# Kernel tuning notes

Measured on AMD Instinct MI355X. Metric: run time of the kernel, lower is better.

Reference implementation:

```python
import jax, jax.numpy as jnp
import numpy as np


def _pick(key, nodes, mask, cnt):
    # Uniformly pick one of the `cnt` entries of `nodes` where mask is True.
    r = jax.random.randint(key, (), 0, jnp.maximum(cnt, 1))
    cs = jnp.cumsum(mask.astype(jnp.int32))
    return nodes[jnp.argmax(cs == r + 1)]


def _one_walk(key, nbrs, f0, n_faces, L):
    # nbrs: [N,3] int32 neighbor table, f0: scalar start face.
    seq = jnp.zeros((L + 1,), jnp.int32).at[0].set(f0)
    visited = jnp.zeros((n_faces + 1,), bool).at[n_faces].set(True).at[f0].set(True)

    def cond(st):
        return st[2] <= L

    def body(st):
        seq, visited, i, bs, k = st
        k, k1, k2, k3 = jax.random.split(k, 4)
        cur = seq[i - 1]
        nb = nbrs[cur]                     # [3] neighbor candidates
        unv = ~visited[nb]
        cnt = unv.sum()
        need = cnt == 0                    # stuck -> backtrack
        cand = _pick(k1, nb, unv, cnt)

        def bcond(c):
            bs_c, found = c[0], c[1]
            return need & (~found) & (i > bs_c)

        def bbody(c):
            bs_c, found, ta, kk = c
            kk, kp = jax.random.split(kk)
            back = seq[i - bs_c - 1]
            bn = nbrs[back]
            bm = ~visited[bn]
            bc = bm.sum()
            f2 = bc > 0
            ta2 = _pick(kp, bn, bm, bc)
            return (jnp.where(f2, bs_c, bs_c + 2), f2, jnp.where(f2, ta2, ta), kk)

        bs_f, found, ta_bt, _ = jax.lax.while_loop(
            bcond, bbody, (bs, jnp.array(False), jnp.int32(0), k2))
        rand_node = jax.random.randint(k3, (), 0, n_faces, dtype=jnp.int32)
        to_add = jnp.where(~need, cand, jnp.where(found, ta_bt, rand_node))
        hit = need & found                 # successful backtrack
        bs_new = jnp.where(hit, bs_f, jnp.int32(1))
        i_new = jnp.where(hit, i - bs_f, i)
        ar = jnp.arange(L + 1, dtype=jnp.int32)
        # torch: replace seq[i-bs:i] with to_add on successful backtrack
        seq = jnp.where(hit & (ar >= i_new) & (ar < i), to_add, seq)
        visited = visited.at[to_add].set(True)
        seq = seq.at[i_new].set(to_add)
        return (seq, visited, i_new + 1, bs_new, k)

    seq, *_ = jax.lax.while_loop(
        cond, body, (seq, visited, jnp.int32(1), jnp.int32(1), key))
    return seq


def patch_random_walk(key, neighbors, centers, n_faces, seq_len):
    B, G = centers.shape
    keys = jax.random.split(key, B * G).reshape(B, G)
    walk_g = jax.vmap(_one_walk, in_axes=(0, None, 0, None, None))
    walk_bg = jax.vmap(walk_g, in_axes=(0, 0, 0, None, None))
    return walk_bg(keys, neighbors, centers, n_faces, seq_len)  # [B,G,L+1] int32


def setup_inputs() -> dict:
    key = jax.random.key(0)
    k1, k2, k3 = jax.random.split(key, 3)
    B, N, G = 4, 20000, 1024
    xyz = jax.random.normal(k1, (B, N, 3), dtype=jnp.float32)
    neighbors = jax.random.randint(k2, (B, N, 3), 0, N, dtype=jnp.int32)
    centers = jax.random.randint(k3, (B, G), 0, N, dtype=jnp.int32)
    return {"xyz": xyz, "neighbors": neighbors, "centers": centers,
            "n_faces": N, "seq_len": 63}


def reference(xyz, neighbors, centers, n_faces, seq_len):
    # patch_random_walk -> idx [B,G,K]; then Group.forward gather + recenter.
    idx = patch_random_walk(jax.random.key(42), neighbors, centers, n_faces, seq_len)
    gather = jax.vmap(lambda p, i: p[i])(xyz, idx)            # [B,G,K,3]
    center_xyz = jax.vmap(lambda p, c: p[c])(xyz, centers)    # [B,G,3]
    return gather - center_xyz[:, :, None, :]
```

## Files before the change

### kernel.cpp

```cpp
#include <hip/hip_runtime.h>
#include <stdint.h>
#include <stddef.h>


namespace {

__device__ __forceinline__ uint32_t rotl32(uint32_t x, int r) {
  return (x << r) | (x >> (32 - r));
}

__device__ __forceinline__ void tf2x32(uint32_t ka, uint32_t kb,
                                       uint32_t x0, uint32_t x1,
                                       uint32_t& o0, uint32_t& o1) {
  const uint32_t kc = ka ^ kb ^ 0x1BD11BDAu;
  x0 += ka; x1 += kb;
#define TF_R4(r0, r1, r2, r3)                          \
  x0 += x1; x1 = rotl32(x1, r0); x1 ^= x0;             \
  x0 += x1; x1 = rotl32(x1, r1); x1 ^= x0;             \
  x0 += x1; x1 = rotl32(x1, r2); x1 ^= x0;             \
  x0 += x1; x1 = rotl32(x1, r3); x1 ^= x0;
  TF_R4(13, 15, 26, 6)  x0 += kb; x1 += kc + 1u;
  TF_R4(17, 29, 16, 24) x0 += kc; x1 += ka + 2u;
  TF_R4(13, 15, 26, 6)  x0 += ka; x1 += kb + 3u;
  TF_R4(17, 29, 16, 24) x0 += kb; x1 += kc + 4u;
  TF_R4(13, 15, 26, 6)  x0 += kc; x1 += ka + 5u;
#undef TF_R4
  o0 = x0; o1 = x1;
}

__device__ __forceinline__ void randbits(uint32_t ka, uint32_t kb,
                                         uint32_t& hi, uint32_t& lo) {
  uint32_t s0a, s0b, s1a, s1b, h0, h1;
  tf2x32(ka, kb, 0u, 0u, s0a, s0b);
  tf2x32(ka, kb, 0u, 1u, s1a, s1b);
  tf2x32(s0a, s0b, 0u, 0u, h0, h1);
  hi = h0 ^ h1;
  tf2x32(s1a, s1b, 0u, 0u, h0, h1);
  lo = h0 ^ h1;
}

__device__ __forceinline__ uint32_t r_generic(uint32_t hi, uint32_t lo,
                                              uint32_t span) {
  uint32_t mult = 65536u % span;
  mult = (mult * mult) % span;
  return ((hi % span) * mult + (lo % span)) % span;
}

__device__ __forceinline__ uint32_t pick_code(uint32_t hi, uint32_t lo) {
  return ((hi % 3u + lo % 3u) % 3u) | ((lo & 1u) << 2);
}

constexpr int WPB = 16;
constexpr int CH = 64;
constexpr int NMAX = 20000;
constexpr int VISW = 625;
constexpr int THREADS = 512;

__global__ __launch_bounds__(512) void walk_kernel(
    const float* __restrict__ xyz, const int* __restrict__ nbrs,
    const int* __restrict__ centers, const int* __restrict__ n_faces_p,
    const int* __restrict__ seq_len_p, float* __restrict__ out,
    int s0, int num_walks, int Lp1) {
  __shared__ uint32_t nb01L[NMAX];
  __shared__ uint16_t nb2L[NMAX];
  __shared__ __align__(16) uint32_t visL[WPB * VISW];
  __shared__ uint16_t seqL[WPB][CH + 4];
  __shared__ float cenL[WPB][3];

  const int tid = threadIdx.x;
  const int wv = tid >> 6, lane = tid & 63;
  const int w0 = blockIdx.x * WPB;
  if (w0 >= num_walks) return;

  const int N = *n_faces_p;
  const int L = *seq_len_p;
  const int B = s0 / (3 * N);
  const int G = num_walks / B;
  const bool lds_ok = (N <= NMAX) && (G % WPB == 0) && (L < CH);
  const int bb0 = w0 / G;

  if (wv == 0) {
    if (lane < WPB && (w0 + lane) < num_walks) {
      uint32_t ka, kb;
      tf2x32(0u, 42u, 0u, (uint32_t)(w0 + lane), ka, kb);
      visL[(lane * CH + 0) * 2 + 0] = ka;
      visL[(lane * CH + 0) * 2 + 1] = kb;
#pragma clang loop unroll(disable)
      for (int c2 = 1; c2 < CH; ++c2) {
        tf2x32(ka, kb, 0u, 0u, ka, kb);
        visL[(lane * CH + c2) * 2 + 0] = ka;
        visL[(lane * CH + c2) * 2 + 1] = kb;
      }
    }
  } else if (lds_ok) {
    const int* __restrict__ nbT = nbrs + (size_t)bb0 * N * 3;
    for (int r = tid - 64; r < N; r += (THREADS - 64)) {
      const int3 v = *reinterpret_cast<const int3*>(nbT + 3 * (size_t)r);
      nb01L[r] = (uint32_t)v.x | ((uint32_t)v.y << 16);
      nb2L[r]  = (uint16_t)v.z;
    }
  }
  __syncthreads();

  if (lds_ok) {
    const float* __restrict__ xb = xyz + (size_t)bb0 * N * 3;
    uint8_t* const codesB = reinterpret_cast<uint8_t*>(&visL[2048]);
#pragma unroll
    for (int p = 0; p < (WPB * CH) / THREADS; ++p) {
      const int pair = tid + THREADS * p;
      const int wk = pair >> 6, st = pair & 63;
      if ((w0 + wk) < num_walks) {
        const uint32_t ka = visL[(wk * CH + st) * 2 + 0];
        const uint32_t kb = visL[(wk * CH + st) * 2 + 1];
        uint32_t k1a, k1b, hi, lo;
        tf2x32(ka, kb, 0u, 1u, k1a, k1b);
        randbits(k1a, k1b, hi, lo);
        codesB[wk * CH + st] = (uint8_t)pick_code(hi, lo);
      }
    }
    if (tid < WPB && (w0 + tid) < num_walks) {
      const int f0t = centers[w0 + tid];
      cenL[tid][0] = xb[3 * (size_t)f0t + 0];
      cenL[tid][1] = xb[3 * (size_t)f0t + 1];
      cenL[tid][2] = xb[3 * (size_t)f0t + 2];
    }
    __syncthreads();

    const int kw = 2 * wv + (lane >> 5);
    const int w = w0 + kw;
    const bool walker = ((lane & 31) == 0) && (w < num_walks);
    uint32_t cw[7] = {0, 0, 0, 0, 0, 0, 0};
    uint32_t k0a = 0, k0b = 0;
    if (walker) {
      tf2x32(0u, 42u, 0u, (uint32_t)w, k0a, k0b);
      const uint32_t* cwd = &visL[2048 + kw * (CH / 4)];
#pragma unroll
      for (int t = 0; t < CH / 4; ++t) {
        const uint32_t wd = cwd[t];
#pragma unroll
        for (int b = 0; b < 4; ++b) {
          const int s = 4 * t + b;
          const uint32_t c3 = (wd >> (8 * b)) & 7u;
          cw[s / 10] |= c3 << (3 * (s % 10));
        }
      }
    }
    __syncthreads();
    {
      uint4* const v4 = reinterpret_cast<uint4*>(visL);
      const uint4 z = make_uint4(0u, 0u, 0u, 0u);
      for (int j = tid; j < (WPB * VISW) / 4; j += THREADS) v4[j] = z;
    }
    __syncthreads();

    const int f0 = walker ? centers[w] : 0;
    uint32_t* __restrict__ visW = visL + (walker ? kw : 0) * VISW;

    if (walker) {
      visW[(unsigned)f0 >> 5] = 1u << (f0 & 31);
      seqL[kw][0] = (uint16_t)f0;
    }

    const uint32_t p0 = nb01L[f0];
    int n0 = (int)(p0 & 0xffffu), n1 = (int)(p0 >> 16), n2 = (int)nb2L[f0];
    uint32_t wd0 = visW[(unsigned)n0 >> 5];
    uint32_t wd1 = visW[(unsigned)n1 >> 5];
    uint32_t wd2 = visW[(unsigned)n2 >> 5];
    uint32_t pA01, pB01, pC01, pA2, pB2, pC2;

    int extc = 0; uint32_t extka = k0a, extkb = k0b;
    int c = 0, bs = 1;
    int i = L + 1;
    bool do_general = true;

    if (L == 63) {
      uint32_t sticky = 0u;
      uint32_t sp[32];
#pragma unroll
      for (int j = 0; j < 32; ++j) sp[j] = 0u;
      sp[0] = (uint32_t)f0 & 0xffffu;
#pragma clang loop unroll(full)
      for (int cc = 0; cc < 63; ++cc) {
        const uint32_t u0 = ((wd0 >> (n0 & 31)) & 1u) ^ 1u;
        const uint32_t u1 = ((wd1 >> (n1 & 31)) & 1u) ^ 1u;
        const uint32_t u2 = ((wd2 >> (n2 & 31)) & 1u) ^ 1u;
        const uint32_t cnt = u0 + u1 + u2;
        sticky |= (cnt == 0u) ? 1u : 0u;
        const uint32_t code = (cw[cc / 10] >> (3 * (cc % 10))) & 7u;
        const uint32_t r3 = code & 3u, r2 = (code >> 2) & 1u;
        const uint32_t tgt = (cnt == 3u ? r3 : (cnt == 2u ? r2 : 0u)) + 1u;
        const int sel = (u0 == tgt) ? 0 : ((u0 + u1 == tgt) ? 1 : 2);
        const int to_add = (sel == 0) ? n0 : ((sel == 1) ? n1 : n2);
        const uint32_t wsel = (sel == 0) ? wd0 : ((sel == 1) ? wd1 : wd2);
        if (walker) {
          visW[(unsigned)to_add >> 5] = wsel | (1u << (to_add & 31));
        }
        sp[(cc + 1) >> 1] |= (uint32_t)to_add << (16 * ((cc + 1) & 1));
        const uint32_t pr01 = nb01L[to_add];
        const uint32_t pr2v = nb2L[to_add];
        n0 = (int)(pr01 & 0xffffu); n1 = (int)(pr01 >> 16); n2 = (int)pr2v;
        wd0 = visW[(unsigned)n0 >> 5];
        wd1 = visW[(unsigned)n1 >> 5];
        wd2 = visW[(unsigned)n2 >> 5];
      }
      if (walker) {
        uint32_t* rowp = reinterpret_cast<uint32_t*>(&seqL[kw][0]);
#pragma unroll
        for (int j = 0; j < 32; ++j) rowp[j] = sp[j];
      }
      const bool redo = walker && (sticky != 0u);
      if (__builtin_expect(__any(redo), 0)) {
        if (redo) {
          for (int j = 0; j < VISW; ++j) visW[j] = 0u;
          visW[(unsigned)f0 >> 5] = 1u << (f0 & 31);
          seqL[kw][0] = (uint16_t)f0;
        }
        i = redo ? 1 : (L + 1);
        c = 0; bs = 1;
        const uint32_t pr0 = nb01L[f0];
        const uint32_t pr2v = nb2L[f0];
        if (redo) {
          n0 = (int)(pr0 & 0xffffu); n1 = (int)(pr0 >> 16); n2 = (int)pr2v;
        }
      } else {
        do_general = false;
      }
    } else {
      i = walker ? 1 : (L + 1);
    }

    if (do_general) {
      pA01 = nb01L[n0]; pA2 = nb2L[n0];
      pB01 = nb01L[n1]; pB2 = nb2L[n1];
      pC01 = nb01L[n2]; pC2 = nb2L[n2];
      wd0 = visW[(unsigned)n0 >> 5];
      wd1 = visW[(unsigned)n1 >> 5];
      wd2 = visW[(unsigned)n2 >> 5];
      for (;; ++c) {
        if (!__any(i <= L)) break;
        const bool act = (i <= L);

        const uint32_t u0 = ((wd0 >> (n0 & 31)) & 1u) ^ 1u;
        const uint32_t u1 = ((wd1 >> (n1 & 31)) & 1u) ^ 1u;
        const uint32_t u2 = ((wd2 >> (n2 & 31)) & 1u) ^ 1u;
        const uint32_t cnt = u0 + u1 + u2;

        uint32_t code;
        if (__builtin_expect(c < CH, 1)) {
          const int wi = c / 10;
          const int sh = 3 * (c - wi * 10);
          uint32_t cwv = cw[0];
          cwv = (wi == 1) ? cw[1] : cwv;  cwv = (wi == 2) ? cw[2] : cwv;
          cwv = (wi == 3) ? cw[3] : cwv;  cwv = (wi == 4) ? cw[4] : cwv;
          cwv = (wi == 5) ? cw[5] : cwv;  cwv = (wi == 6) ? cw[6] : cwv;
          code = (cwv >> sh) & 7u;
        } else {
          while (extc < c) { tf2x32(extka, extkb, 0u, 0u, extka, extkb); ++extc; }
          uint32_t k1a, k1b, hi, lo;
          tf2x32(extka, extkb, 0u, 1u, k1a, k1b);
          randbits(k1a, k1b, hi, lo);
          code = pick_code(hi, lo);
        }

        const bool need = act && (cnt == 0u);
        if (__builtin_expect(__any(need), 0)) {
          while (extc < c) { tf2x32(extka, extkb, 0u, 0u, extka, extkb); ++extc; }
          const uint32_t kia = extka, kib = extkb;
          bool found = false; int ta = 0; int bsc = bs;
          if (need) {
            uint32_t kka, kkb;
            tf2x32(kia, kib, 0u, 2u, kka, kkb);
            while (!found && i > bsc) {
              uint32_t ca, cb, kpa, kpb;
              tf2x32(kka, kkb, 0u, 0u, ca, cb);
              tf2x32(kka, kkb, 0u, 1u, kpa, kpb);
              const int back = (int)seqL[kw][i - bsc - 1];
              const uint32_t pm = nb01L[back];
              const int m0 = (int)(pm & 0xffffu), m1 = (int)(pm >> 16);
              const int m2 = (int)nb2L[back];
              const uint32_t e0 = ((visW[(unsigned)m0 >> 5] >> (m0 & 31)) & 1u) ^ 1u;
              const uint32_t e1 = ((visW[(unsigned)m1 >> 5] >> (m1 & 31)) & 1u) ^ 1u;
              const uint32_t e2 = ((visW[(unsigned)m2 >> 5] >> (m2 & 31)) & 1u) ^ 1u;
              const uint32_t bc = e0 + e1 + e2;
              if (bc > 0) {
                uint32_t bhi, blo;
                randbits(kpa, kpb, bhi, blo);
                const uint32_t bcode = pick_code(bhi, blo);
                const uint32_t br3 = bcode & 3u, br2 = (bcode >> 2) & 1u;
                const uint32_t t2v = (bc == 3 ? br3 : (bc == 2 ? br2 : 0)) + 1;
                ta = (e0 == t2v) ? m0 : ((e0 + e1 == t2v) ? m1 : m2);
                found = true;
              } else {
                bsc += 2;
              }
              kka = ca; kkb = cb;
            }
          }
          int rnd = 0;
          if (need && !found) {
            uint32_t k3a, k3b, rhi, rlo;
            tf2x32(kia, kib, 0u, 3u, k3a, k3b);
            randbits(k3a, k3b, rhi, rlo);
            rnd = (int)r_generic(rhi, rlo, (uint32_t)N);
          }
          const uint32_t r3 = code & 3u, r2 = (code >> 2) & 1u;
          const uint32_t tgt = (cnt == 3 ? r3 : (cnt == 2 ? r2 : 0)) + 1;
          const int selc = (u0 == tgt) ? 0 : ((u0 + u1 == tgt) ? 1 : 2);
          const int to_add_c = (selc == 0) ? n0 : ((selc == 1) ? n1 : n2);
          const uint32_t wselc = (selc == 0) ? wd0 : ((selc == 1) ? wd1 : wd2);

          const bool hit = need && found;
          const int to_add = need ? (found ? ta : rnd) : to_add_c;

          if (act) {
            uint32_t wdf = need ? visW[(unsigned)to_add >> 5] : wselc;
            visW[(unsigned)to_add >> 5] = wdf | (1u << (to_add & 31));
            if (hit) {
              const int i_new = i - bsc;
              for (int j = i_new; j < i; ++j) seqL[kw][j] = (uint16_t)to_add;
              bs = bsc; i = i_new + 1;
            } else {
              seqL[kw][i] = (uint16_t)to_add;
              bs = 1; ++i;
            }
          }
          const int rn = act ? to_add : 0;
          const uint32_t pr = nb01L[rn];
          const uint32_t pr2 = nb2L[rn];
          if (act) {
            n0 = (int)(pr & 0xffffu); n1 = (int)(pr >> 16); n2 = (int)pr2;
          }
        } else {
          const uint32_t r3 = code & 3u, r2 = (code >> 2) & 1u;
          const uint32_t tgt = (cnt == 3 ? r3 : (cnt == 2 ? r2 : 0)) + 1;
          const int sel = (u0 == tgt) ? 0 : ((u0 + u1 == tgt) ? 1 : 2);
          const int to_add = (sel == 0) ? n0 : ((sel == 1) ? n1 : n2);
          const uint32_t wsel = (sel == 0) ? wd0 : ((sel == 1) ? wd1 : wd2);
          if (act) {
            visW[(unsigned)to_add >> 5] = wsel | (1u << (to_add & 31));
            seqL[kw][i] = (uint16_t)to_add;
            bs = 1; ++i;
            if (sel == 0)      { n0 = (int)(pA01 & 0xffffu); n1 = (int)(pA01 >> 16); n2 = (int)pA2; }
            else if (sel == 1) { n0 = (int)(pB01 & 0xffffu); n1 = (int)(pB01 >> 16); n2 = (int)pB2; }
            else               { n0 = (int)(pC01 & 0xffffu); n1 = (int)(pC01 >> 16); n2 = (int)pC2; }
          }
        }
        pA01 = nb01L[n0]; pA2 = nb2L[n0];
        pB01 = nb01L[n1]; pB2 = nb2L[n1];
        pC01 = nb01L[n2]; pC2 = nb2L[n2];
        wd0 = visW[(unsigned)n0 >> 5];
        wd1 = visW[(unsigned)n1 >> 5];
        wd2 = visW[(unsigned)n2 >> 5];
      }
    }

    __syncthreads();

    const int items = WPB * Lp1;
    for (int idx = tid; idx < items; idx += THREADS) {
      const int wl = idx / Lp1;
      const int p = idx - wl * Lp1;
      const int ww = w0 + wl;
      if (ww < num_walks) {
        const int node = (int)seqL[wl][p];
        const float* xr = xb + 3 * (size_t)node;
        float3 v;
        v.x = xr[0] - cenL[wl][0];
        v.y = xr[1] - cenL[wl][1];
        v.z = xr[2] - cenL[wl][2];
        *reinterpret_cast<float3*>(out + ((size_t)ww * Lp1 + p) * 3) = v;
      }
    }
  } else {
    for (int sub = 0; sub < 2; ++sub) {
      const int w = w0 + 2 * wv + sub;
      if (w >= num_walks) continue;
      const int bb = w / G;
      const int* __restrict__ nbG = nbrs + (size_t)bb * N * 3;
      const float* __restrict__ xb = xyz + (size_t)bb * N * 3;
      const int f0 = centers[w];
      const uint32_t mka = visL[((2 * wv + sub) * CH + lane) * 2 + 0];
      const uint32_t mkb = visL[((2 * wv + sub) * CH + lane) * 2 + 1];
      uint32_t mycode;
      {
        uint32_t k1a, k1b, hi, lo;
        tf2x32(mka, mkb, 0u, 1u, k1a, k1b);
        randbits(k1a, k1b, hi, lo);
        mycode = pick_code(hi, lo);
      }
      uint32_t extka = 0, extkb = 0;
      int extc = -1;
      auto get_key = [&](int idxk, uint32_t& ra, uint32_t& rb) {
        if (idxk < CH) {
          ra = (uint32_t)__shfl((int)mka, idxk);
          rb = (uint32_t)__shfl((int)mkb, idxk);
        } else {
          if (extc < 0) {
            extka = (uint32_t)__shfl((int)mka, CH - 1);
            extkb = (uint32_t)__shfl((int)mkb, CH - 1);
            extc = CH - 1;
          }
          while (extc < idxk) { tf2x32(extka, extkb, 0u, 0u, extka, extkb); ++extc; }
          ra = extka; rb = extkb;
        }
      };

      int seqr = (lane == 0) ? f0 : -1;
      uint32_t code_next = (uint32_t)__shfl((int)mycode, 0);
      int i = 1, bs = 1, c = 0;
      int hist  = (lane == 0) ? f0 : -1;
      int hist2 = -1;
      int3 row = *reinterpret_cast<const int3*>(nbG + 3 * (size_t)f0);
      while (i <= L) {
        const int idx = c; ++c;
        const bool deep = (idx >= CH);
        const uint32_t codeP = code_next;
        code_next = (uint32_t)__shfl((int)mycode, (c < CH) ? c : 0);

        const int n0 = row.x, n1 = row.y, n2 = row.z;
        int v0 = __any(hist == n0), v1 = __any(hist == n1), v2 = __any(hist == n2);
        if (deep) {
          v0 |= __any(hist2 == n0); v1 |= __any(hist2 == n1); v2 |= __any(hist2 == n2);
        }
        const int u0 = 1 - v0, u1 = 1 - v1, u2 = 1 - v2;
        const int cnt = u0 + u1 + u2;

        int to_add;
        bool hit = false;
        int bsf = bs;
        if (cnt > 0) {
          uint32_t code = codeP;
          if (deep) {
            uint32_t ia, ib, k1a, k1b, hi, lo;
            get_key(idx, ia, ib);
            tf2x32(ia, ib, 0u, 1u, k1a, k1b);
            randbits(k1a, k1b, hi, lo);
            code = pick_code(hi, lo);
          }
          const int r3 = (int)(code & 3u), r2 = (int)((code >> 2) & 1u);
          const int target = (cnt == 3 ? r3 : (cnt == 2 ? r2 : 0)) + 1;
          to_add = (u0 == target) ? n0 : ((u0 + u1 == target) ? n1 : n2);
        } else {
          uint32_t kia, kib;
          get_key(idx, kia, kib);
          uint32_t kka, kkb;
          tf2x32(kia, kib, 0u, 2u, kka, kkb);
          bool found = false;
          int ta = 0, bsc = bs;
          while (!found && i > bsc) {
            uint32_t ca, cb, kpa, kpb;
            tf2x32(kka, kkb, 0u, 0u, ca, cb);
            tf2x32(kka, kkb, 0u, 1u, kpa, kpb);
            const int back = __shfl(seqr, i - bsc - 1);
            const int3 br = *reinterpret_cast<const int3*>(nbG + 3 * (size_t)back);
            int w0m = __any(hist == br.x), w1m = __any(hist == br.y), w2m = __any(hist == br.z);
            if (deep) {
              w0m |= __any(hist2 == br.x); w1m |= __any(hist2 == br.y); w2m |= __any(hist2 == br.z);
            }
            const int e0 = 1 - w0m, e1 = 1 - w1m, e2 = 1 - w2m;
            const int bc = e0 + e1 + e2;
            if (bc > 0) {
              uint32_t bhi, blo;
              randbits(kpa, kpb, bhi, blo);
              const uint32_t bcode = pick_code(bhi, blo);
              const int r3 = (int)(bcode & 3u), r2 = (int)((bcode >> 2) & 1u);
              const int t2v = (bc == 3 ? r3 : (bc == 2 ? r2 : 0)) + 1;
              ta = (e0 == t2v) ? br.x : ((e0 + e1 == t2v) ? br.y : br.z);
              found = true;
            } else {
              bsc += 2;
            }
            kka = ca; kkb = cb;
          }
          if (found) {
            to_add = ta; hit = true; bsf = bsc;
          } else {
            uint32_t k3a, k3b, rhi, rlo;
            tf2x32(kia, kib, 0u, 3u, k3a, k3b);
            randbits(k3a, k3b, rhi, rlo);
            to_add = (int)r_generic(rhi, rlo, (uint32_t)N);
          }
        }

        int i_new, up;
        if (hit) { i_new = i - bsf; bs = bsf; up = i - 1; }
        else     { i_new = i;       bs = 1;   up = i; }
        seqr = (lane >= i_new && lane <= up) ? to_add : seqr;

        const int slot = idx + 1;
        if (slot < CH)          hist  = (lane == slot)      ? to_add : hist;
        else if (slot < 2 * CH) hist2 = (lane == slot - CH) ? to_add : hist2;

        i = i_new + 1;
        row = *reinterpret_cast<const int3*>(nbG + 3 * (size_t)to_add);
      }

      const float cx = xb[3 * (size_t)f0 + 0];
      const float cy = xb[3 * (size_t)f0 + 1];
      const float cz = xb[3 * (size_t)f0 + 2];
      if (lane < Lp1) {
        const int node = seqr;
        float3 v;
        v.x = xb[3 * (size_t)node + 0] - cx;
        v.y = xb[3 * (size_t)node + 1] - cy;
        v.z = xb[3 * (size_t)node + 2] - cz;
        *reinterpret_cast<float3*>(out + ((size_t)w * Lp1 + lane) * 3) = v;
      }
    }
  }
}

}

extern "C" void kernel_launch(void* const* d_in, const int* in_sizes, int n_in,
                              void* d_out, int out_size, void* d_ws, size_t ws_size,
                              hipStream_t stream) {
  const float* xyz     = (const float*)d_in[0];
  const int*   nbrs    = (const int*)d_in[1];
  const int*   centers = (const int*)d_in[2];
  const int*   n_faces = (const int*)d_in[3];
  const int*   seq_len = (const int*)d_in[4];
  float* out = (float*)d_out;

  const int s0 = in_sizes[0];
  const int num_walks = in_sizes[2];
  const int Lp1 = out_size / (3 * num_walks);

  const int blocks = (num_walks + WPB - 1) / WPB;
  walk_kernel<<<blocks, THREADS, 0, stream>>>(
      xyz, nbrs, centers, n_faces, seq_len, out, s0, num_walks, Lp1);
}
```

Measured before the change: 88.74 us.

## Overlap random-code generation with walker execution via LDS spin-wait producer wave

In the fast path, wave 0 now produces the per-step pick codes into a dedicated shared buffer while waves 1-7 run the walks at the same time. Walkers poll the buffer with volatile reads, spinning until the 0xFF sentinel is overwritten. Previously codes were computed in a separate phase behind several barriers. The visited-bitmap clear and neighbor-table staging now happen in the same initial phase, which removes extra __syncthreads. The risk is busy-wait stalls if the producer falls behind, and uneven walker distribution across waves (3,3,2,2,2,2,2).

```diff
diff --git a/kernel.cpp b/kernel.cpp
--- a/kernel.cpp
+++ b/kernel.cpp
@@ -66,6 +66,9 @@
   __shared__ __align__(16) uint32_t visL[WPB * VISW];
   __shared__ uint16_t seqL[WPB][CH + 4];
   __shared__ float cenL[WPB][3];
+  __shared__ uint32_t codesW[(WPB * CH) / 4];
+
+  uint8_t* const codesB = reinterpret_cast<uint8_t*>(codesW);
 
   const int tid = threadIdx.x;
   const int wv = tid >> 6, lane = tid & 63;
@@ -79,299 +82,23 @@
   const bool lds_ok = (N <= NMAX) && (G % WPB == 0) && (L < CH);
   const int bb0 = w0 / G;
 
-  if (wv == 0) {
-    if (lane < WPB && (w0 + lane) < num_walks) {
-      uint32_t ka, kb;
-      tf2x32(0u, 42u, 0u, (uint32_t)(w0 + lane), ka, kb);
-      visL[(lane * CH + 0) * 2 + 0] = ka;
-      visL[(lane * CH + 0) * 2 + 1] = kb;
+  if (!lds_ok) {
+    if (wv == 0) {
+      if (lane < WPB && (w0 + lane) < num_walks) {
+        uint32_t ka, kb;
+        tf2x32(0u, 42u, 0u, (uint32_t)(w0 + lane), ka, kb);
+        visL[(lane * CH + 0) * 2 + 0] = ka;
+        visL[(lane * CH + 0) * 2 + 1] = kb;
 #pragma clang loop unroll(disable)
-      for (int c2 = 1; c2 < CH; ++c2) {
-        tf2x32(ka, kb, 0u, 0u, ka, kb);
-        visL[(lane * CH + c2) * 2 + 0] = ka;
-        visL[(lane * CH + c2) * 2 + 1] = kb;
-      }
-    }
-  } else if (lds_ok) {
-    const int* __restrict__ nbT = nbrs + (size_t)bb0 * N * 3;
-    for (int r = tid - 64; r < N; r += (THREADS - 64)) {
-      const int3 v = *reinterpret_cast<const int3*>(nbT + 3 * (size_t)r);
-      nb01L[r] = (uint32_t)v.x | ((uint32_t)v.y << 16);
-      nb2L[r]  = (uint16_t)v.z;
-    }
-  }
-  __syncthreads();
-
-  if (lds_ok) {
-    const float* __restrict__ xb = xyz + (size_t)bb0 * N * 3;
-    uint8_t* const codesB = reinterpret_cast<uint8_t*>(&visL[2048]);
-#pragma unroll
-    for (int p = 0; p < (WPB * CH) / THREADS; ++p) {
-      const int pair = tid + THREADS * p;
-      const int wk = pair >> 6, st = pair & 63;
-      if ((w0 + wk) < num_walks) {
-        const uint32_t ka = visL[(wk * CH + st) * 2 + 0];
-        const uint32_t kb = visL[(wk * CH + st) * 2 + 1];
-        uint32_t k1a, k1b, hi, lo;
-        tf2x32(ka, kb, 0u, 1u, k1a, k1b);
-        randbits(k1a, k1b, hi, lo);
-        codesB[wk * CH + st] = (uint8_t)pick_code(hi, lo);
-      }
-    }
-    if (tid < WPB && (w0 + tid) < num_walks) {
-      const int f0t = centers[w0 + tid];
-      cenL[tid][0] = xb[3 * (size_t)f0t + 0];
-      cenL[tid][1] = xb[3 * (size_t)f0t + 1];
-      cenL[tid][2] = xb[3 * (size_t)f0t + 2];
+        for (int c2 = 1; c2 < CH; ++c2) {
+          tf2x32(ka, kb, 0u, 0u, ka, kb);
+          visL[(lane * CH + c2) * 2 + 0] = ka;
+          visL[(lane * CH + c2) * 2 + 1] = kb;
+        }
+      }
     }
     __syncthreads();
 
-    const int kw = 2 * wv + (lane >> 5);
-    const int w = w0 + kw;
-    const bool walker = ((lane & 31) == 0) && (w < num_walks);
-    uint32_t cw[7] = {0, 0, 0, 0, 0, 0, 0};
-    uint32_t k0a = 0, k0b = 0;
-    if (walker) {
-      tf2x32(0u, 42u, 0u, (uint32_t)w, k0a, k0b);
-      const uint32_t* cwd = &visL[2048 + kw * (CH / 4)];
-#pragma unroll
-      for (int t = 0; t < CH / 4; ++t) {
-        const uint32_t wd = cwd[t];
-#pragma unroll
-        for (int b = 0; b < 4; ++b) {
-          const int s = 4 * t + b;
-          const uint32_t c3 = (wd >> (8 * b)) & 7u;
-          cw[s / 10] |= c3 << (3 * (s % 10));
-        }
-      }
-    }
-    __syncthreads();
-    {
-      uint4* const v4 = reinterpret_cast<uint4*>(visL);
-      const uint4 z = make_uint4(0u, 0u, 0u, 0u);
-      for (int j = tid; j < (WPB * VISW) / 4; j += THREADS) v4[j] = z;
-    }
-    __syncthreads();
-
-    const int f0 = walker ? centers[w] : 0;
-    uint32_t* __restrict__ visW = visL + (walker ? kw : 0) * VISW;
-
-    if (walker) {
-      visW[(unsigned)f0 >> 5] = 1u << (f0 & 31);
-      seqL[kw][0] = (uint16_t)f0;
-    }
-
-    const uint32_t p0 = nb01L[f0];
-    int n0 = (int)(p0 & 0xffffu), n1 = (int)(p0 >> 16), n2 = (int)nb2L[f0];
-    uint32_t wd0 = visW[(unsigned)n0 >> 5];
-    uint32_t wd1 = visW[(unsigned)n1 >> 5];
-    uint32_t wd2 = visW[(unsigned)n2 >> 5];
-    uint32_t pA01, pB01, pC01, pA2, pB2, pC2;
-
-    int extc = 0; uint32_t extka = k0a, extkb = k0b;
-    int c = 0, bs = 1;
-    int i = L + 1;
-    bool do_general = true;
-
-    if (L == 63) {
-      uint32_t sticky = 0u;
-      uint32_t sp[32];
-#pragma unroll
-      for (int j = 0; j < 32; ++j) sp[j] = 0u;
-      sp[0] = (uint32_t)f0 & 0xffffu;
-#pragma clang loop unroll(full)
-      for (int cc = 0; cc < 63; ++cc) {
-        const uint32_t u0 = ((wd0 >> (n0 & 31)) & 1u) ^ 1u;
-        const uint32_t u1 = ((wd1 >> (n1 & 31)) & 1u) ^ 1u;
-        const uint32_t u2 = ((wd2 >> (n2 & 31)) & 1u) ^ 1u;
-        const uint32_t cnt = u0 + u1 + u2;
-        sticky |= (cnt == 0u) ? 1u : 0u;
-        const uint32_t code = (cw[cc / 10] >> (3 * (cc % 10))) & 7u;
-        const uint32_t r3 = code & 3u, r2 = (code >> 2) & 1u;
-        const uint32_t tgt = (cnt == 3u ? r3 : (cnt == 2u ? r2 : 0u)) + 1u;
-        const int sel = (u0 == tgt) ? 0 : ((u0 + u1 == tgt) ? 1 : 2);
-        const int to_add = (sel == 0) ? n0 : ((sel == 1) ? n1 : n2);
-        const uint32_t wsel = (sel == 0) ? wd0 : ((sel == 1) ? wd1 : wd2);
-        if (walker) {
-          visW[(unsigned)to_add >> 5] = wsel | (1u << (to_add & 31));
-        }
-        sp[(cc + 1) >> 1] |= (uint32_t)to_add << (16 * ((cc + 1) & 1));
-        const uint32_t pr01 = nb01L[to_add];
-        const uint32_t pr2v = nb2L[to_add];
-        n0 = (int)(pr01 & 0xffffu); n1 = (int)(pr01 >> 16); n2 = (int)pr2v;
-        wd0 = visW[(unsigned)n0 >> 5];
-        wd1 = visW[(unsigned)n1 >> 5];
-        wd2 = visW[(unsigned)n2 >> 5];
-      }
-      if (walker) {
-        uint32_t* rowp = reinterpret_cast<uint32_t*>(&seqL[kw][0]);
-#pragma unroll
-        for (int j = 0; j < 32; ++j) rowp[j] = sp[j];
-      }
-      const bool redo = walker && (sticky != 0u);
-      if (__builtin_expect(__any(redo), 0)) {
-        if (redo) {
-          for (int j = 0; j < VISW; ++j) visW[j] = 0u;
-          visW[(unsigned)f0 >> 5] = 1u << (f0 & 31);
-          seqL[kw][0] = (uint16_t)f0;
-        }
-        i = redo ? 1 : (L + 1);
-        c = 0; bs = 1;
-        const uint32_t pr0 = nb01L[f0];
-        const uint32_t pr2v = nb2L[f0];
-        if (redo) {
-          n0 = (int)(pr0 & 0xffffu); n1 = (int)(pr0 >> 16); n2 = (int)pr2v;
-        }
-      } else {
-        do_general = false;
-      }
-    } else {
-      i = walker ? 1 : (L + 1);
-    }
-
-    if (do_general) {
-      pA01 = nb01L[n0]; pA2 = nb2L[n0];
-      pB01 = nb01L[n1]; pB2 = nb2L[n1];
-      pC01 = nb01L[n2]; pC2 = nb2L[n2];
-      wd0 = visW[(unsigned)n0 >> 5];
-      wd1 = visW[(unsigned)n1 >> 5];
-      wd2 = visW[(unsigned)n2 >> 5];
-      for (;; ++c) {
-        if (!__any(i <= L)) break;
-        const bool act = (i <= L);
-
-        const uint32_t u0 = ((wd0 >> (n0 & 31)) & 1u) ^ 1u;
-        const uint32_t u1 = ((wd1 >> (n1 & 31)) & 1u) ^ 1u;
-        const uint32_t u2 = ((wd2 >> (n2 & 31)) & 1u) ^ 1u;
-        const uint32_t cnt = u0 + u1 + u2;
-
-        uint32_t code;
-        if (__builtin_expect(c < CH, 1)) {
-          const int wi = c / 10;
-          const int sh = 3 * (c - wi * 10);
-          uint32_t cwv = cw[0];
-          cwv = (wi == 1) ? cw[1] : cwv;  cwv = (wi == 2) ? cw[2] : cwv;
-          cwv = (wi == 3) ? cw[3] : cwv;  cwv = (wi == 4) ? cw[4] : cwv;
-          cwv = (wi == 5) ? cw[5] : cwv;  cwv = (wi == 6) ? cw[6] : cwv;
-          code = (cwv >> sh) & 7u;
-        } else {
-          while (extc < c) { tf2x32(extka, extkb, 0u, 0u, extka, extkb); ++extc; }
-          uint32_t k1a, k1b, hi, lo;
-          tf2x32(extka, extkb, 0u, 1u, k1a, k1b);
-          randbits(k1a, k1b, hi, lo);
-          code = pick_code(hi, lo);
-        }
-
-        const bool need = act && (cnt == 0u);
-        if (__builtin_expect(__any(need), 0)) {
-          while (extc < c) { tf2x32(extka, extkb, 0u, 0u, extka, extkb); ++extc; }
-          const uint32_t kia = extka, kib = extkb;
-          bool found = false; int ta = 0; int bsc = bs;
-          if (need) {
-            uint32_t kka, kkb;
-            tf2x32(kia, kib, 0u, 2u, kka, kkb);
-            while (!found && i > bsc) {
-              uint32_t ca, cb, kpa, kpb;
-              tf2x32(kka, kkb, 0u, 0u, ca, cb);
-              tf2x32(kka, kkb, 0u, 1u, kpa, kpb);
-              const int back = (int)seqL[kw][i - bsc - 1];
-              const uint32_t pm = nb01L[back];
-              const int m0 = (int)(pm & 0xffffu), m1 = (int)(pm >> 16);
-              const int m2 = (int)nb2L[back];
-              const uint32_t e0 = ((visW[(unsigned)m0 >> 5] >> (m0 & 31)) & 1u) ^ 1u;
-              const uint32_t e1 = ((visW[(unsigned)m1 >> 5] >> (m1 & 31)) & 1u) ^ 1u;
-              const uint32_t e2 = ((visW[(unsigned)m2 >> 5] >> (m2 & 31)) & 1u) ^ 1u;
-              const uint32_t bc = e0 + e1 + e2;
-              if (bc > 0) {
-                uint32_t bhi, blo;
-                randbits(kpa, kpb, bhi, blo);
-                const uint32_t bcode = pick_code(bhi, blo);
-                const uint32_t br3 = bcode & 3u, br2 = (bcode >> 2) & 1u;
-                const uint32_t t2v = (bc == 3 ? br3 : (bc == 2 ? br2 : 0)) + 1;
-                ta = (e0 == t2v) ? m0 : ((e0 + e1 == t2v) ? m1 : m2);
-                found = true;
-              } else {
-                bsc += 2;
-              }
-              kka = ca; kkb = cb;
-            }
-          }
-          int rnd = 0;
-          if (need && !found) {
-            uint32_t k3a, k3b, rhi, rlo;
-            tf2x32(kia, kib, 0u, 3u, k3a, k3b);
-            randbits(k3a, k3b, rhi, rlo);
-            rnd = (int)r_generic(rhi, rlo, (uint32_t)N);
-          }
-          const uint32_t r3 = code & 3u, r2 = (code >> 2) & 1u;
-          const uint32_t tgt = (cnt == 3 ? r3 : (cnt == 2 ? r2 : 0)) + 1;
-          const int selc = (u0 == tgt) ? 0 : ((u0 + u1 == tgt) ? 1 : 2);
-          const int to_add_c = (selc == 0) ? n0 : ((selc == 1) ? n1 : n2);
-          const uint32_t wselc = (selc == 0) ? wd0 : ((selc == 1) ? wd1 : wd2);
-
-          const bool hit = need && found;
-          const int to_add = need ? (found ? ta : rnd) : to_add_c;
-
-          if (act) {
-            uint32_t wdf = need ? visW[(unsigned)to_add >> 5] : wselc;
-            visW[(unsigned)to_add >> 5] = wdf | (1u << (to_add & 31));
-            if (hit) {
-              const int i_new = i - bsc;
-              for (int j = i_new; j < i; ++j) seqL[kw][j] = (uint16_t)to_add;
-              bs = bsc; i = i_new + 1;
-            } else {
-              seqL[kw][i] = (uint16_t)to_add;
-              bs = 1; ++i;
-            }
-          }
-          const int rn = act ? to_add : 0;
-          const uint32_t pr = nb01L[rn];
-          const uint32_t pr2 = nb2L[rn];
-          if (act) {
-            n0 = (int)(pr & 0xffffu); n1 = (int)(pr >> 16); n2 = (int)pr2;
-          }
-        } else {
-          const uint32_t r3 = code & 3u, r2 = (code >> 2) & 1u;
-          const uint32_t tgt = (cnt == 3 ? r3 : (cnt == 2 ? r2 : 0)) + 1;
-          const int sel = (u0 == tgt) ? 0 : ((u0 + u1 == tgt) ? 1 : 2);
-          const int to_add = (sel == 0) ? n0 : ((sel == 1) ? n1 : n2);
-          const uint32_t wsel = (sel == 0) ? wd0 : ((sel == 1) ? wd1 : wd2);
-          if (act) {
-            visW[(unsigned)to_add >> 5] = wsel | (1u << (to_add & 31));
-            seqL[kw][i] = (uint16_t)to_add;
-            bs = 1; ++i;
-            if (sel == 0)      { n0 = (int)(pA01 & 0xffffu); n1 = (int)(pA01 >> 16); n2 = (int)pA2; }
-            else if (sel == 1) { n0 = (int)(pB01 & 0xffffu); n1 = (int)(pB01 >> 16); n2 = (int)pB2; }
-            else               { n0 = (int)(pC01 & 0xffffu); n1 = (int)(pC01 >> 16); n2 = (int)pC2; }
-          }
-        }
-        pA01 = nb01L[n0]; pA2 = nb2L[n0];
-        pB01 = nb01L[n1]; pB2 = nb2L[n1];
-        pC01 = nb01L[n2]; pC2 = nb2L[n2];
-        wd0 = visW[(unsigned)n0 >> 5];
-        wd1 = visW[(unsigned)n1 >> 5];
-        wd2 = visW[(unsigned)n2 >> 5];
-      }
-    }
-
-    __syncthreads();
-
-    const int items = WPB * Lp1;
-    for (int idx = tid; idx < items; idx += THREADS) {
-      const int wl = idx / Lp1;
-      const int p = idx - wl * Lp1;
-      const int ww = w0 + wl;
-      if (ww < num_walks) {
-        const int node = (int)seqL[wl][p];
-        const float* xr = xb + 3 * (size_t)node;
-        float3 v;
-        v.x = xr[0] - cenL[wl][0];
-        v.y = xr[1] - cenL[wl][1];
-        v.z = xr[2] - cenL[wl][2];
-        *reinterpret_cast<float3*>(out + ((size_t)ww * Lp1 + p) * 3) = v;
-      }
-    }
-  } else {
     for (int sub = 0; sub < 2; ++sub) {
       const int w = w0 + 2 * wv + sub;
       if (w >= num_walks) continue;
@@ -507,6 +234,292 @@
         *reinterpret_cast<float3*>(out + ((size_t)w * Lp1 + lane) * 3) = v;
       }
     }
+    return;
+  }
+
+  const float* __restrict__ xb = xyz + (size_t)bb0 * N * 3;
+
+  if (wv == 0) {
+    for (int j = lane; j < (WPB * CH) / 4; j += 64) codesW[j] = 0xFFFFFFFFu;
+  } else {
+    const int* __restrict__ nbT = nbrs + (size_t)bb0 * N * 3;
+    for (int r = tid - 64; r < N; r += (THREADS - 64)) {
+      const int3 v = *reinterpret_cast<const int3*>(nbT + 3 * (size_t)r);
+      nb01L[r] = (uint32_t)v.x | ((uint32_t)v.y << 16);
+      nb2L[r]  = (uint16_t)v.z;
+    }
+    if (tid >= 64 && tid < 64 + WPB && (w0 + tid - 64) < num_walks) {
+      const int f0t = centers[w0 + tid - 64];
+      cenL[tid - 64][0] = xb[3 * (size_t)f0t + 0];
+      cenL[tid - 64][1] = xb[3 * (size_t)f0t + 1];
+      cenL[tid - 64][2] = xb[3 * (size_t)f0t + 2];
+    }
+    {
+      uint4* const v4 = reinterpret_cast<uint4*>(visL);
+      const uint4 z = make_uint4(0u, 0u, 0u, 0u);
+      for (int j = tid - 64; j < (WPB * VISW) / 4; j += (THREADS - 64)) v4[j] = z;
+    }
+  }
+  __syncthreads();
+
+  if (wv == 0) {
+    const int pw = lane & 15;
+    const int sub = lane >> 4;
+    const bool pok = (w0 + pw) < num_walks;
+    uint32_t ka, kb;
+    tf2x32(0u, 42u, 0u, (uint32_t)(w0 + pw), ka, kb);
+#pragma clang loop unroll(disable)
+    for (int rnd = 0; rnd < CH / 4; ++rnd) {
+      const uint32_t s0a = ka, s0b = kb;
+      tf2x32(ka, kb, 0u, 0u, ka, kb);
+      const uint32_t s1a = ka, s1b = kb;
+      tf2x32(ka, kb, 0u, 0u, ka, kb);
+      const uint32_t s2a = ka, s2b = kb;
+      tf2x32(ka, kb, 0u, 0u, ka, kb);
+      const uint32_t s3a = ka, s3b = kb;
+      tf2x32(ka, kb, 0u, 0u, ka, kb);
+      uint32_t mka = s0a, mkb = s0b;
+      mka = (sub == 1) ? s1a : mka;  mkb = (sub == 1) ? s1b : mkb;
+      mka = (sub == 2) ? s2a : mka;  mkb = (sub == 2) ? s2b : mkb;
+      mka = (sub == 3) ? s3a : mka;  mkb = (sub == 3) ? s3b : mkb;
+      uint32_t k1a, k1b, hi, lo;
+      tf2x32(mka, mkb, 0u, 1u, k1a, k1b);
+      randbits(k1a, k1b, hi, lo);
+      const uint32_t code = pick_code(hi, lo);
+      if (pok) codesB[pw * CH + (4 * rnd + sub)] = (uint8_t)code;
+    }
+  } else {
+    const int nw = (wv <= 2) ? 3 : 2;
+    int s = -1;
+    if (nw == 3) s = (lane == 0) ? 0 : ((lane == 21) ? 1 : ((lane == 42) ? 2 : -1));
+    else         s = (lane == 0) ? 0 : ((lane == 32) ? 1 : -1);
+    const int kw0 = (wv <= 2) ? 3 * (wv - 1) : 6 + 2 * (wv - 3);
+    const int kw = (s >= 0) ? (kw0 + s) : 0;
+    const int w = w0 + ((s >= 0) ? kw : 0);
+    const bool walker = (s >= 0) && (w < num_walks);
+
+    volatile const uint8_t* cbv = codesB;
+    auto get_code = [&](int cc) -> uint32_t {
+      uint32_t v = cbv[kw * CH + cc];
+      while (__builtin_expect(v == 0xFFu, 0)) v = cbv[kw * CH + cc];
+      return v & 7u;
+    };
+
+    const int f0 = walker ? centers[w] : 0;
+    uint32_t* __restrict__ visW = visL + kw * VISW;
+
+    uint32_t k0a, k0b;
+    tf2x32(0u, 42u, 0u, (uint32_t)w, k0a, k0b);
+
+    if (walker) {
+      visW[(unsigned)f0 >> 5] = 1u << (f0 & 31);
+      seqL[kw][0] = (uint16_t)f0;
+    }
+
+    const uint32_t p0 = nb01L[f0];
+    int n0 = (int)(p0 & 0xffffu), n1 = (int)(p0 >> 16), n2 = (int)nb2L[f0];
+    uint32_t wd0 = visW[(unsigned)n0 >> 5];
+    uint32_t wd1 = visW[(unsigned)n1 >> 5];
+    uint32_t wd2 = visW[(unsigned)n2 >> 5];
+    uint32_t pA01, pB01, pC01, pA2, pB2, pC2;
+
+    int extc = 0; uint32_t extka = k0a, extkb = k0b;
+    int c = 0, bs = 1;
+    int i = L + 1;
+    bool do_general = true;
+
+    if (L == 63) {
+      uint32_t sticky = 0u;
+      uint32_t sp[32];
+#pragma unroll
+      for (int j = 0; j < 32; ++j) sp[j] = 0u;
+      sp[0] = (uint32_t)f0 & 0xffffu;
+#pragma clang loop unroll(full)
+      for (int cc = 0; cc < 63; ++cc) {
+        const uint32_t u0 = ((wd0 >> (n0 & 31)) & 1u) ^ 1u;
+        const uint32_t u1 = ((wd1 >> (n1 & 31)) & 1u) ^ 1u;
+        const uint32_t u2 = ((wd2 >> (n2 & 31)) & 1u) ^ 1u;
+        const uint32_t cnt = u0 + u1 + u2;
+        sticky |= (cnt == 0u) ? 1u : 0u;
+        const uint32_t code = get_code(cc);
+        const uint32_t r3 = code & 3u, r2 = (code >> 2) & 1u;
+        const uint32_t tgt = (cnt == 3u ? r3 : (cnt == 2u ? r2 : 0u)) + 1u;
+        const int sel = (u0 == tgt) ? 0 : ((u0 + u1 == tgt) ? 1 : 2);
+        const int to_add = (sel == 0) ? n0 : ((sel == 1) ? n1 : n2);
+        const uint32_t wsel = (sel == 0) ? wd0 : ((sel == 1) ? wd1 : wd2);
+        if (walker) {
+          visW[(unsigned)to_add >> 5] = wsel | (1u << (to_add & 31));
+        }
+        sp[(cc + 1) >> 1] |= (uint32_t)to_add << (16 * ((cc + 1) & 1));
+        const uint32_t pr01 = nb01L[to_add];
+        const uint32_t pr2v = nb2L[to_add];
+        n0 = (int)(pr01 & 0xffffu); n1 = (int)(pr01 >> 16); n2 = (int)pr2v;
+        wd0 = visW[(unsigned)n0 >> 5];
+        wd1 = visW[(unsigned)n1 >> 5];
+        wd2 = visW[(unsigned)n2 >> 5];
+      }
+      if (walker) {
+        uint32_t* rowp = reinterpret_cast<uint32_t*>(&seqL[kw][0]);
+#pragma unroll
+        for (int j = 0; j < 32; ++j) rowp[j] = sp[j];
+      }
+      const bool redo = walker && (sticky != 0u);
+      if (__builtin_expect(__any(redo), 0)) {
+        if (redo) {
+          for (int j = 0; j < VISW; ++j) visW[j] = 0u;
+          visW[(unsigned)f0 >> 5] = 1u << (f0 & 31);
+          seqL[kw][0] = (uint16_t)f0;
+        }
+        i = redo ? 1 : (L + 1);
+        c = 0; bs = 1;
+        const uint32_t pr0 = nb01L[f0];
+        const uint32_t pr2v = nb2L[f0];
+        if (redo) {
+          n0 = (int)(pr0 & 0xffffu); n1 = (int)(pr0 >> 16); n2 = (int)pr2v;
+        }
+      } else {
+        do_general = false;
+      }
+    } else {
+      i = walker ? 1 : (L + 1);
+    }
+
+    if (do_general) {
+      pA01 = nb01L[n0]; pA2 = nb2L[n0];
+      pB01 = nb01L[n1]; pB2 = nb2L[n1];
+      pC01 = nb01L[n2]; pC2 = nb2L[n2];
+      wd0 = visW[(unsigned)n0 >> 5];
+      wd1 = visW[(unsigned)n1 >> 5];
+      wd2 = visW[(unsigned)n2 >> 5];
+      for (;; ++c) {
+        if (!__any(i <= L)) break;
+        const bool act = (i <= L);
+
+        const uint32_t u0 = ((wd0 >> (n0 & 31)) & 1u) ^ 1u;
+        const uint32_t u1 = ((wd1 >> (n1 & 31)) & 1u) ^ 1u;
+        const uint32_t u2 = ((wd2 >> (n2 & 31)) & 1u) ^ 1u;
+        const uint32_t cnt = u0 + u1 + u2;
+
+        uint32_t code;
+        if (__builtin_expect(c < CH, 1)) {
+          code = get_code(c);
+        } else {
+          while (extc < c) { tf2x32(extka, extkb, 0u, 0u, extka, extkb); ++extc; }
+          uint32_t k1a, k1b, hi, lo;
+          tf2x32(extka, extkb, 0u, 1u, k1a, k1b);
+          randbits(k1a, k1b, hi, lo);
+          code = pick_code(hi, lo);
+        }
+
+        const bool need = act && (cnt == 0u);
+        if (__builtin_expect(__any(need), 0)) {
+          while (extc < c) { tf2x32(extka, extkb, 0u, 0u, extka, extkb); ++extc; }
+          const uint32_t kia = extka, kib = extkb;
+          bool found = false; int ta = 0; int bsc = bs;
+          if (need) {
+            uint32_t kka, kkb;
+            tf2x32(kia, kib, 0u, 2u, kka, kkb);
+            while (!found && i > bsc) {
+              uint32_t ca, cb, kpa, kpb;
+              tf2x32(kka, kkb, 0u, 0u, ca, cb);
+              tf2x32(kka, kkb, 0u, 1u, kpa, kpb);
+              const int back = (int)seqL[kw][i - bsc - 1];
+              const uint32_t pm = nb01L[back];
+              const int m0 = (int)(pm & 0xffffu), m1 = (int)(pm >> 16);
+              const int m2 = (int)nb2L[back];
+              const uint32_t e0 = ((visW[(unsigned)m0 >> 5] >> (m0 & 31)) & 1u) ^ 1u;
+              const uint32_t e1 = ((visW[(unsigned)m1 >> 5] >> (m1 & 31)) & 1u) ^ 1u;
+              const uint32_t e2 = ((visW[(unsigned)m2 >> 5] >> (m2 & 31)) & 1u) ^ 1u;
+              const uint32_t bc = e0 + e1 + e2;
+              if (bc > 0) {
+                uint32_t bhi, blo;
+                randbits(kpa, kpb, bhi, blo);
+                const uint32_t bcode = pick_code(bhi, blo);
+                const uint32_t br3 = bcode & 3u, br2 = (bcode >> 2) & 1u;
+                const uint32_t t2v = (bc == 3 ? br3 : (bc == 2 ? br2 : 0)) + 1;
+                ta = (e0 == t2v) ? m0 : ((e0 + e1 == t2v) ? m1 : m2);
+                found = true;
+              } else {
+                bsc += 2;
+              }
+              kka = ca; kkb = cb;
+            }
+          }
+          int rnd = 0;
+          if (need && !found) {
+            uint32_t k3a, k3b, rhi, rlo;
+            tf2x32(kia, kib, 0u, 3u, k3a, k3b);
+            randbits(k3a, k3b, rhi, rlo);
+            rnd = (int)r_generic(rhi, rlo, (uint32_t)N);
+          }
+          const uint32_t r3 = code & 3u, r2 = (code >> 2) & 1u;
+          const uint32_t tgt = (cnt == 3 ? r3 : (cnt == 2 ? r2 : 0)) + 1;
+          const int selc = (u0 == tgt) ? 0 : ((u0 + u1 == tgt) ? 1 : 2);
+          const int to_add_c = (selc == 0) ? n0 : ((selc == 1) ? n1 : n2);
+          const uint32_t wselc = (selc == 0) ? wd0 : ((selc == 1) ? wd1 : wd2);
+
+          const bool hit = need && found;
+          const int to_add = need ? (found ? ta : rnd) : to_add_c;
+
+          if (act) {
+            uint32_t wdf = need ? visW[(unsigned)to_add >> 5] : wselc;
+            visW[(unsigned)to_add >> 5] = wdf | (1u << (to_add & 31));
+            if (hit) {
+              const int i_new = i - bsc;
+              for (int j = i_new; j < i; ++j) seqL[kw][j] = (uint16_t)to_add;
+              bs = bsc; i = i_new + 1;
+            } else {
+              seqL[kw][i] = (uint16_t)to_add;
+              bs = 1; ++i;
+            }
+          }
+          const int rn = act ? to_add : 0;
+          const uint32_t pr = nb01L[rn];
+          const uint32_t pr2 = nb2L[rn];
+          if (act) {
+            n0 = (int)(pr & 0xffffu); n1 = (int)(pr >> 16); n2 = (int)pr2;
+          }
+        } else {
+          const uint32_t r3 = code & 3u, r2 = (code >> 2) & 1u;
+          const uint32_t tgt = (cnt == 3 ? r3 : (cnt == 2 ? r2 : 0)) + 1;
+          const int sel = (u0 == tgt) ? 0 : ((u0 + u1 == tgt) ? 1 : 2);
+          const int to_add = (sel == 0) ? n0 : ((sel == 1) ? n1 : n2);
+          const uint32_t wsel = (sel == 0) ? wd0 : ((sel == 1) ? wd1 : wd2);
+          if (act) {
+            visW[(unsigned)to_add >> 5] = wsel | (1u << (to_add & 31));
+            seqL[kw][i] = (uint16_t)to_add;
+            bs = 1; ++i;
+            if (sel == 0)      { n0 = (int)(pA01 & 0xffffu); n1 = (int)(pA01 >> 16); n2 = (int)pA2; }
+            else if (sel == 1) { n0 = (int)(pB01 & 0xffffu); n1 = (int)(pB01 >> 16); n2 = (int)pB2; }
+            else               { n0 = (int)(pC01 & 0xffffu); n1 = (int)(pC01 >> 16); n2 = (int)pC2; }
+          }
+        }
+        pA01 = nb01L[n0]; pA2 = nb2L[n0];
+        pB01 = nb01L[n1]; pB2 = nb2L[n1];
+        pC01 = nb01L[n2]; pC2 = nb2L[n2];
+        wd0 = visW[(unsigned)n0 >> 5];
+        wd1 = visW[(unsigned)n1 >> 5];
+        wd2 = visW[(unsigned)n2 >> 5];
+      }
+    }
+  }
+
+  __syncthreads();
+
+  const int items = WPB * Lp1;
+  for (int idx = tid; idx < items; idx += THREADS) {
+    const int wl = idx / Lp1;
+    const int p = idx - wl * Lp1;
+    const int ww = w0 + wl;
+    if (ww < num_walks) {
+      const int node = (int)seqL[wl][p];
+      const float* xr = xb + 3 * (size_t)node;
+      float3 v;
+      v.x = xr[0] - cenL[wl][0];
+      v.y = xr[1] - cenL[wl][1];
+      v.z = xr[2] - cenL[wl][2];
+      *reinterpret_cast<float3*>(out + ((size_t)ww * Lp1 + p) * 3) = v;
+    }
   }
 }
 
```

Measured after the change: 97.63 us. 10.0% more time.
